# Kernel optimization log

Measured on AMD Instinct MI355X. Metric: run time of the kernel, lower is better.

Reference implementation:

```python
import jax, jax.numpy as jnp
import numpy as np

B, D, K, U = 4096, 1024, 5, 1024  # batch, input_dim, num_basis, units


def setup_inputs() -> dict:
    key = jax.random.key(0)
    k1, k2, k3 = jax.random.split(key, 3)
    x = jax.random.normal(k1, (B, D), dtype=jnp.float32)
    basis_weights = jax.random.normal(k2, (D, K, U), dtype=jnp.float32) * 0.02
    bias = jax.random.normal(k3, (U,), dtype=jnp.float32) * 0.02
    return {"x": x, "basis_weights": basis_weights, "bias": bias}


def reference(x, basis_weights, bias):
    # Polynomial basis expansion: x^0, x^1, ..., x^{K-1}  -> (B, D, K)
    num_basis = basis_weights.shape[1]
    powers = jnp.arange(num_basis, dtype=x.dtype)
    basis = x[..., None] ** powers  # x**0 == 1, matching tf.ones_like branch
    # Fused: einsum('bik,ikj->bij') followed by reduce_sum over i == 'bik,ikj->bj'.
    # Avoids materializing the (B, D, U) intermediate of the original.
    out = jnp.einsum("bik,ikj->bj", basis, basis_weights) + bias
    # tf.nn.gelu defaults to exact (non-approximate) GELU.
    return jax.nn.gelu(out, approximate=False)
```

## Files before the change

### kernel.cpp

```cpp
#include <hip/hip_runtime.h>
#include <hip/hip_bf16.h>
#include <math.h>


#define B_DIM 4096
#define D_DIM 1024
#define U_DIM 1024
#define KT2 4096
#define NKB 128

typedef unsigned short ushort_t;
typedef __attribute__((ext_vector_type(8))) short bf16x8;
typedef __attribute__((ext_vector_type(4))) float f32x4;

__device__ __forceinline__ ushort_t f2bf(float f) {
  union { float f; unsigned int u; } v;
  v.f = f;
  unsigned int r = v.u + 0x7FFFu + ((v.u >> 16) & 1u);
  return (ushort_t)(r >> 16);
}

__device__ __forceinline__ void load_lds16(const ushort_t* g, ushort_t* l) {
  __builtin_amdgcn_global_load_lds(
      (const __attribute__((address_space(1))) ushort_t*)g,
      (__attribute__((address_space(3))) ushort_t*)l, 16, 0, 0);
}

__device__ __forceinline__ float gelu_exact(float v) {
  return 0.5f * v * (1.0f + erff(v * 0.70710678118654752f));
}


__global__ __launch_bounds__(256) void prep_kernel(
    const float* __restrict__ x, const float* __restrict__ W,
    const float* __restrict__ bias, ushort_t* __restrict__ Ap,
    ushort_t* __restrict__ Bp, float* __restrict__ b2) {
  __shared__ __align__(16) float lsh[16][260];

  const int bid  = blockIdx.x;
  const int t    = threadIdx.x;
  const int wave = t >> 6;
  const int lane = t & 63;
  const int m    = lane & 15;
  const int ko   = lane >> 4;

  if (bid < 1024) {
    const int bx  = bid & 3;
    const int m16 = bid >> 2;
    const float* xbase = x + (size_t)m16 * 16 * D_DIM + bx * 256;
#pragma unroll
    for (int p = 0; p < 4; ++p) {
      const int row = p * 4 + wave;
      const int c4  = lane;
      *(float4*)&lsh[row][c4 * 4] =
          *(const float4*)(xbase + (size_t)row * D_DIM + c4 * 4);
    }
    __syncthreads();
#pragma unroll
    for (int u = 0; u < 8; ++u) {
      const int kl  = u * 4 + wave;
      const int col = kl * 8 + ko * 2;
      const float xa = lsh[m][col], xb = lsh[m][col + 1];
      const float xa2 = xa * xa, xb2 = xb * xb;
      ushort_t o[8];
      o[0] = f2bf(xa);  o[1] = f2bf(xa2);
      o[2] = f2bf(xa2 * xa); o[3] = f2bf(xa2 * xa2);
      o[4] = f2bf(xb);  o[5] = f2bf(xb2);
      o[6] = f2bf(xb2 * xb); o[7] = f2bf(xb2 * xb2);
      *(uint4*)(Ap + ((size_t)m16 * NKB + bx * 32 + kl) * 512 + lane * 8) =
          *(const uint4*)o;
    }
  } else {
    const int n16 = bid - 1024;
    const int j   = n16 * 16 + m;
    float s0 = 0.0f;
#pragma unroll 2
    for (int it2 = 0; it2 < 32; ++it2) {
      const int kblk = it2 * 4 + wave;
      const int i0   = kblk * 8 + ko * 2;
      ushort_t o[8];
#pragma unroll
      for (int t2 = 0; t2 < 2; ++t2) {
        const int i = i0 + t2;
        s0 += W[(size_t)(i * 5) * U_DIM + j];
#pragma unroll
        for (int e = 0; e < 4; ++e)
          o[t2 * 4 + e] = f2bf(W[(size_t)(i * 5 + e + 1) * U_DIM + j]);
      }
      *(uint4*)(Bp + ((size_t)n16 * NKB + kblk) * 512 + lane * 8) =
          *(const uint4*)o;
    }
    s0 += __shfl_xor(s0, 16, 64);
    s0 += __shfl_xor(s0, 32, 64);
    float* red = &lsh[0][0];
    __syncthreads();
    if (ko == 0) red[wave * 16 + m] = s0;
    __syncthreads();
    if (wave == 0 && ko == 0)
      b2[j] = bias[j] + red[m] + red[16 + m] + red[32 + m] + red[48 + m];
  }
}

__global__ __launch_bounds__(256) void gemm_kernel(
    const ushort_t* __restrict__ Ap, const ushort_t* __restrict__ Bp,
    const float* __restrict__ b2, float* __restrict__ C) {
  __shared__ __align__(16) ushort_t lds[4][12 * 512];

  const int tid  = threadIdx.x;
  const int wave = tid >> 6;
  const int lane = tid & 63;
  const int wm   = wave >> 1;
  const int wn   = wave & 1;

  const int lin  = blockIdx.y * 8 + blockIdx.x;
  const int xcd  = lin & 7;
  const int slot = lin >> 3;
  const int mt   = xcd * 8 + (slot & 7);
  const int nt   = slot >> 3;
  const int m16b = mt * 4;
  const int n16b = nt * 8;

  const ushort_t* gcur[3];
  int ldst[3];
#pragma unroll
  for (int s = 0; s < 3; ++s) {
    const int u = s * 4 + wave;
    const ushort_t* base = (u < 4)
        ? Ap + ((size_t)(m16b + u) * NKB) * 512
        : Bp + ((size_t)(n16b + (u - 4)) * NKB) * 512;
    gcur[s] = base + lane * 8;
    ldst[s] = u * 512 + lane * 8;
  }

  f32x4 acc[2][4];
  const f32x4 zero = {0.0f, 0.0f, 0.0f, 0.0f};
#pragma unroll
  for (int mf = 0; mf < 2; ++mf)
#pragma unroll
    for (int nf = 0; nf < 4; ++nf) acc[mf][nf] = zero;

#define WAITBAR(N) \
  asm volatile("s_waitcnt vmcnt(" #N ")\n\ts_barrier" ::: "memory")

#define STAGE_REL(bb, rel)                                              \
  do {                                                                  \
    _Pragma("unroll")                                                   \
    for (int s = 0; s < 3; ++s)                                         \
      load_lds16(gcur[s] + (rel) * 512, &lds[bb][ldst[s]]);             \
  } while (0)

#define COMPUTE(bb)                                                     \
  do {                                                                  \
    bf16x8 a[2], b[4];                                                  \
    _Pragma("unroll")                                                   \
    for (int mf = 0; mf < 2; ++mf)                                      \
      a[mf] = *(const bf16x8*)&lds[bb][(wm * 2 + mf) * 512 + lane * 8]; \
    _Pragma("unroll")                                                   \
    for (int nf = 0; nf < 4; ++nf)                                      \
      b[nf] = *(const bf16x8*)&lds[bb][(4 + wn * 4 + nf) * 512 + lane * 8]; \
    _Pragma("unroll")                                                   \
    for (int mf = 0; mf < 2; ++mf)                                      \
      _Pragma("unroll")                                                 \
      for (int nf = 0; nf < 4; ++nf)                                    \
        acc[mf][nf] = __builtin_amdgcn_mfma_f32_16x16x32_bf16(          \
            a[mf], b[nf], acc[mf][nf], 0, 0, 0);                        \
  } while (0)

  STAGE_REL(0, 0);
  STAGE_REL(1, 1);
  STAGE_REL(2, 2);
#pragma unroll
  for (int s = 0; s < 3; ++s) gcur[s] += 4 * 512;

  for (int base = 0; base < 124; base += 4) {
    WAITBAR(6); STAGE_REL(3, -1); COMPUTE(0);
    WAITBAR(6); STAGE_REL(0,  0); COMPUTE(1);
    WAITBAR(6); STAGE_REL(1,  1); COMPUTE(2);
    WAITBAR(6); STAGE_REL(2,  2); COMPUTE(3);
#pragma unroll
    for (int s = 0; s < 3; ++s) gcur[s] += 4 * 512;
  }
  WAITBAR(6); STAGE_REL(3, -1); COMPUTE(0);
  WAITBAR(6); COMPUTE(1);
  WAITBAR(3); COMPUTE(2);
  WAITBAR(0); COMPUTE(3);
#undef STAGE_REL
#undef COMPUTE
#undef WAITBAR

  const int crow0 = m16b * 16 + wm * 32 + (lane >> 4) * 4;
  const int ccol0 = n16b * 16 + wn * 64 + (lane & 15);
#pragma unroll
  for (int nf = 0; nf < 4; ++nf) {
    const int col = ccol0 + nf * 16;
    const float bv = b2[col];
#pragma unroll
    for (int mf = 0; mf < 2; ++mf) {
#pragma unroll
      for (int r = 0; r < 4; ++r) {
        const int row = crow0 + mf * 16 + r;
        C[(size_t)row * U_DIM + col] = gelu_exact(acc[mf][nf][r] + bv);
      }
    }
  }
}

__global__ void fallback_kernel(const float* __restrict__ x, const float* __restrict__ W,
                                const float* __restrict__ bias, float* __restrict__ out) {
  int j  = blockIdx.x * 256 + threadIdx.x;
  int b0 = blockIdx.y * 16;
  float acc[16];
#pragma unroll
  for (int t = 0; t < 16; ++t) acc[t] = 0.0f;
  for (int i = 0; i < D_DIM; ++i) {
    const float* wr = W + (size_t)i * 5 * U_DIM + j;
    float w0 = wr[0 * U_DIM], w1 = wr[1 * U_DIM], w2 = wr[2 * U_DIM];
    float w3 = wr[3 * U_DIM], w4 = wr[4 * U_DIM];
#pragma unroll
    for (int t = 0; t < 16; ++t) {
      float xv = x[(size_t)(b0 + t) * D_DIM + i];
      float x2 = xv * xv;
      acc[t] += w0 + xv * w1 + x2 * w2 + x2 * xv * w3 + x2 * x2 * w4;
    }
  }
  float bv = bias[j];
#pragma unroll
  for (int t = 0; t < 16; ++t)
    out[(size_t)(b0 + t) * U_DIM + j] = gelu_exact(acc[t] + bv);
}

extern "C" void kernel_launch(void* const* d_in, const int* in_sizes, int n_in,
                              void* d_out, int out_size, void* d_ws, size_t ws_size,
                              hipStream_t stream) {
  const float* x    = (const float*)d_in[0];
  const float* W    = (const float*)d_in[1];
  const float* bias = (const float*)d_in[2];
  float* out = (float*)d_out;

  const size_t szA = (size_t)B_DIM * KT2 * sizeof(ushort_t);
  const size_t szB = (size_t)U_DIM * KT2 * sizeof(ushort_t);
  const size_t szb = (size_t)U_DIM * sizeof(float);

  if (ws_size >= szA + szB + szb) {
    ushort_t* Ap = (ushort_t*)d_ws;
    ushort_t* Bp = (ushort_t*)((char*)d_ws + szA);
    float*    b2 = (float*)((char*)d_ws + szA + szB);
    prep_kernel<<<dim3(1024 + 64), 256, 0, stream>>>(x, W, bias, Ap, Bp, b2);
    gemm_kernel<<<dim3(U_DIM / 128, B_DIM / 64), 256, 0, stream>>>(Ap, Bp, b2, out);
  } else {
    fallback_kernel<<<dim3(U_DIM / 256, B_DIM / 16), 256, 0, stream>>>(x, W, bias, out);
  }
}
```

Before: 138.2 us.

## Compute polynomial powers of x inside GEMM instead of materializing bf16 A

The prep kernel now only relayouts x as fp32 into the MFMA fragment order. The GEMM loads two fp32 values per lane and computes x, x^2, x^3, x^4 and their bf16 packing on the fly, which shrinks the prep write and GEMM read of A from a 4x-expanded bf16 buffer to fp32 x. The W repack is split across 8 k-groups for more parallelism, with partial row-0 sums folded into the bias inside the GEMM epilogue. The cost is extra VALU work per MFMA step inside the GEMM main loop and a per-lane LDS read pattern that may cause bank conflicts.

Result: slower. 149.6 us (+8.2%).

```diff
diff --git a/kernel.cpp b/kernel.cpp
--- a/kernel.cpp
+++ b/kernel.cpp
@@ -6,12 +6,12 @@
 #define B_DIM 4096
 #define D_DIM 1024
 #define U_DIM 1024
-#define KT2 4096
 #define NKB 128
 
 typedef unsigned short ushort_t;
 typedef __attribute__((ext_vector_type(8))) short bf16x8;
 typedef __attribute__((ext_vector_type(4))) float f32x4;
+typedef __attribute__((ext_vector_type(2))) float f32x2;
 
 __device__ __forceinline__ ushort_t f2bf(float f) {
   union { float f; unsigned int u; } v;
@@ -33,9 +33,9 @@
 
 __global__ __launch_bounds__(256) void prep_kernel(
     const float* __restrict__ x, const float* __restrict__ W,
-    const float* __restrict__ bias, ushort_t* __restrict__ Ap,
-    ushort_t* __restrict__ Bp, float* __restrict__ b2) {
-  __shared__ __align__(16) float lsh[16][260];
+    float* __restrict__ Xp, ushort_t* __restrict__ Bp,
+    float* __restrict__ fold8) {
+  __shared__ __align__(16) float lsh[64][132];
 
   const int bid  = blockIdx.x;
   const int t    = threadIdx.x;
@@ -44,39 +44,38 @@
   const int m    = lane & 15;
   const int ko   = lane >> 4;
 
-  if (bid < 1024) {
-    const int bx  = bid & 3;
-    const int m16 = bid >> 2;
-    const float* xbase = x + (size_t)m16 * 16 * D_DIM + bx * 256;
-#pragma unroll
-    for (int p = 0; p < 4; ++p) {
-      const int row = p * 4 + wave;
-      const int c4  = lane;
+  if (bid < 512) {
+    const int mt = bid >> 3;
+    const int g  = bid & 7;
+    const float* xbase = x + (size_t)mt * 64 * D_DIM + g * 128;
+#pragma unroll
+    for (int p = 0; p < 8; ++p) {
+      const int row = p * 8 + wave * 2 + (lane >> 5);
+      const int c4  = lane & 31;
       *(float4*)&lsh[row][c4 * 4] =
           *(const float4*)(xbase + (size_t)row * D_DIM + c4 * 4);
     }
     __syncthreads();
 #pragma unroll
-    for (int u = 0; u < 8; ++u) {
-      const int kl  = u * 4 + wave;
-      const int col = kl * 8 + ko * 2;
-      const float xa = lsh[m][col], xb = lsh[m][col + 1];
-      const float xa2 = xa * xa, xb2 = xb * xb;
-      ushort_t o[8];
-      o[0] = f2bf(xa);  o[1] = f2bf(xa2);
-      o[2] = f2bf(xa2 * xa); o[3] = f2bf(xa2 * xa2);
-      o[4] = f2bf(xb);  o[5] = f2bf(xb2);
-      o[6] = f2bf(xb2 * xb); o[7] = f2bf(xb2 * xb2);
-      *(uint4*)(Ap + ((size_t)m16 * NKB + bx * 32 + kl) * 512 + lane * 8) =
-          *(const uint4*)o;
+    for (int r = 0; r < 4; ++r) {
+      const int itl = r * 4 + wave;
+      const int it  = g * 16 + itl;
+      float* dst = Xp + ((size_t)(mt * NKB + it)) * 512 + lane * 8;
+      float f[8];
+#pragma unroll
+      for (int j = 0; j < 8; ++j) f[j] = lsh[lane][itl * 8 + j];
+      *(float4*)(dst)     = *(const float4*)&f[0];
+      *(float4*)(dst + 4) = *(const float4*)&f[4];
     }
   } else {
-    const int n16 = bid - 1024;
+    const int wid = bid - 512;
+    const int n16 = wid >> 3;
+    const int kg  = wid & 7;
     const int j   = n16 * 16 + m;
     float s0 = 0.0f;
-#pragma unroll 2
-    for (int it2 = 0; it2 < 32; ++it2) {
-      const int kblk = it2 * 4 + wave;
+#pragma unroll
+    for (int kk = 0; kk < 4; ++kk) {
+      const int kblk = kg * 16 + kk * 4 + wave;
       const int i0   = kblk * 8 + ko * 2;
       ushort_t o[8];
 #pragma unroll
@@ -93,18 +92,19 @@
     s0 += __shfl_xor(s0, 16, 64);
     s0 += __shfl_xor(s0, 32, 64);
     float* red = &lsh[0][0];
-    __syncthreads();
     if (ko == 0) red[wave * 16 + m] = s0;
     __syncthreads();
     if (wave == 0 && ko == 0)
-      b2[j] = bias[j] + red[m] + red[16 + m] + red[32 + m] + red[48 + m];
+      fold8[(size_t)kg * U_DIM + j] =
+          red[m] + red[16 + m] + red[32 + m] + red[48 + m];
   }
 }
 
 __global__ __launch_bounds__(256) void gemm_kernel(
-    const ushort_t* __restrict__ Ap, const ushort_t* __restrict__ Bp,
-    const float* __restrict__ b2, float* __restrict__ C) {
-  __shared__ __align__(16) ushort_t lds[4][12 * 512];
+    const float* __restrict__ Xp, const ushort_t* __restrict__ Bp,
+    const float* __restrict__ bias, const float* __restrict__ fold8,
+    float* __restrict__ C) {
+  __shared__ __align__(16) ushort_t lds[4][5120];
 
   const int tid  = threadIdx.x;
   const int wave = tid >> 6;
@@ -120,17 +120,13 @@
   const int m16b = mt * 4;
   const int n16b = nt * 8;
 
-  const ushort_t* gcur[3];
-  int ldst[3];
-#pragma unroll
-  for (int s = 0; s < 3; ++s) {
-    const int u = s * 4 + wave;
-    const ushort_t* base = (u < 4)
-        ? Ap + ((size_t)(m16b + u) * NKB) * 512
-        : Bp + ((size_t)(n16b + (u - 4)) * NKB) * 512;
-    gcur[s] = base + lane * 8;
-    ldst[s] = u * 512 + lane * 8;
-  }
+  const ushort_t* gx  = (const ushort_t*)(Xp + (size_t)mt * NKB * 512) + lane * 8;
+  const ushort_t* gb0 = Bp + ((size_t)(n16b + wave) * NKB) * 512 + lane * 8;
+  const ushort_t* gb1 = Bp + ((size_t)(n16b + 4 + wave) * NKB) * 512 + lane * 8;
+  const int ldx0 = lane * 8;
+  const int ldx1 = 512 + lane * 8;
+  const int ldb0 = 1024 + wave * 512 + lane * 8;
+  const int ldb1 = 1024 + (4 + wave) * 512 + lane * 8;
 
   f32x4 acc[2][4];
   const f32x4 zero = {0.0f, 0.0f, 0.0f, 0.0f};
@@ -144,20 +140,37 @@
 
 #define STAGE_REL(bb, rel)                                              \
   do {                                                                  \
-    _Pragma("unroll")                                                   \
-    for (int s = 0; s < 3; ++s)                                         \
-      load_lds16(gcur[s] + (rel) * 512, &lds[bb][ldst[s]]);             \
+    load_lds16(gx  + (rel) * 1024,       &lds[bb][ldx0]);               \
+    load_lds16(gx  + (rel) * 1024 + 512, &lds[bb][ldx1]);               \
+    load_lds16(gb0 + (rel) * 512,        &lds[bb][ldb0]);               \
+    load_lds16(gb1 + (rel) * 512,        &lds[bb][ldb1]);               \
+  } while (0)
+
+#define PACKA(dst, xp)                                                  \
+  do {                                                                  \
+    const f32x2 p1 = (xp);                                              \
+    const f32x2 p2 = p1 * p1;                                           \
+    const f32x2 p3 = p2 * p1;                                           \
+    const f32x2 p4 = p2 * p2;                                           \
+    bf16x8 rr;                                                          \
+    rr[0] = (short)f2bf(p1[0]); rr[1] = (short)f2bf(p2[0]);             \
+    rr[2] = (short)f2bf(p3[0]); rr[3] = (short)f2bf(p4[0]);             \
+    rr[4] = (short)f2bf(p1[1]); rr[5] = (short)f2bf(p2[1]);             \
+    rr[6] = (short)f2bf(p3[1]); rr[7] = (short)f2bf(p4[1]);             \
+    dst = rr;                                                           \
   } while (0)
 
 #define COMPUTE(bb)                                                     \
   do {                                                                  \
+    const float* xu = (const float*)&lds[bb][0];                        \
+    f32x2 xp0 = *(const f32x2*)&xu[((wm * 2 + 0) * 16 + (lane & 15)) * 8 + (lane >> 4) * 2]; \
+    f32x2 xp1 = *(const f32x2*)&xu[((wm * 2 + 1) * 16 + (lane & 15)) * 8 + (lane >> 4) * 2]; \
     bf16x8 a[2], b[4];                                                  \
-    _Pragma("unroll")                                                   \
-    for (int mf = 0; mf < 2; ++mf)                                      \
-      a[mf] = *(const bf16x8*)&lds[bb][(wm * 2 + mf) * 512 + lane * 8]; \
+    PACKA(a[0], xp0);                                                   \
+    PACKA(a[1], xp1);                                                   \
     _Pragma("unroll")                                                   \
     for (int nf = 0; nf < 4; ++nf)                                      \
-      b[nf] = *(const bf16x8*)&lds[bb][(4 + wn * 4 + nf) * 512 + lane * 8]; \
+      b[nf] = *(const bf16x8*)&lds[bb][1024 + (wn * 4 + nf) * 512 + lane * 8]; \
     _Pragma("unroll")                                                   \
     for (int mf = 0; mf < 2; ++mf)                                      \
       _Pragma("unroll")                                                 \
@@ -169,23 +182,26 @@
   STAGE_REL(0, 0);
   STAGE_REL(1, 1);
   STAGE_REL(2, 2);
-#pragma unroll
-  for (int s = 0; s < 3; ++s) gcur[s] += 4 * 512;
+  gx  += 4 * 1024;
+  gb0 += 4 * 512;
+  gb1 += 4 * 512;
 
   for (int base = 0; base < 124; base += 4) {
-    WAITBAR(6); STAGE_REL(3, -1); COMPUTE(0);
-    WAITBAR(6); STAGE_REL(0,  0); COMPUTE(1);
-    WAITBAR(6); STAGE_REL(1,  1); COMPUTE(2);
-    WAITBAR(6); STAGE_REL(2,  2); COMPUTE(3);
-#pragma unroll
-    for (int s = 0; s < 3; ++s) gcur[s] += 4 * 512;
-  }
-  WAITBAR(6); STAGE_REL(3, -1); COMPUTE(0);
-  WAITBAR(6); COMPUTE(1);
-  WAITBAR(3); COMPUTE(2);
+    WAITBAR(8); STAGE_REL(3, -1); COMPUTE(0);
+    WAITBAR(8); STAGE_REL(0,  0); COMPUTE(1);
+    WAITBAR(8); STAGE_REL(1,  1); COMPUTE(2);
+    WAITBAR(8); STAGE_REL(2,  2); COMPUTE(3);
+    gx  += 4 * 1024;
+    gb0 += 4 * 512;
+    gb1 += 4 * 512;
+  }
+  WAITBAR(8); STAGE_REL(3, -1); COMPUTE(0);
+  WAITBAR(8); COMPUTE(1);
+  WAITBAR(4); COMPUTE(2);
   WAITBAR(0); COMPUTE(3);
 #undef STAGE_REL
 #undef COMPUTE
+#undef PACKA
 #undef WAITBAR
 
   const int crow0 = m16b * 16 + wm * 32 + (lane >> 4) * 4;
@@ -193,7 +209,9 @@
 #pragma unroll
   for (int nf = 0; nf < 4; ++nf) {
     const int col = ccol0 + nf * 16;
-    const float bv = b2[col];
+    float bv = bias[col];
+#pragma unroll
+    for (int kg = 0; kg < 8; ++kg) bv += fold8[(size_t)kg * U_DIM + col];
 #pragma unroll
     for (int mf = 0; mf < 2; ++mf) {
 #pragma unroll
@@ -237,16 +255,16 @@
   const float* bias = (const float*)d_in[2];
   float* out = (float*)d_out;
 
-  const size_t szA = (size_t)B_DIM * KT2 * sizeof(ushort_t);
-  const size_t szB = (size_t)U_DIM * KT2 * sizeof(ushort_t);
-  const size_t szb = (size_t)U_DIM * sizeof(float);
-
-  if (ws_size >= szA + szB + szb) {
-    ushort_t* Ap = (ushort_t*)d_ws;
-    ushort_t* Bp = (ushort_t*)((char*)d_ws + szA);
-    float*    b2 = (float*)((char*)d_ws + szA + szB);
-    prep_kernel<<<dim3(1024 + 64), 256, 0, stream>>>(x, W, bias, Ap, Bp, b2);
-    gemm_kernel<<<dim3(U_DIM / 128, B_DIM / 64), 256, 0, stream>>>(Ap, Bp, b2, out);
+  const size_t szX = (size_t)B_DIM * D_DIM * sizeof(float);
+  const size_t szB = (size_t)U_DIM * 4096 * sizeof(ushort_t);
+  const size_t szF = (size_t)8 * U_DIM * sizeof(float);
+
+  if (ws_size >= szX + szB + szF) {
+    float*    Xp = (float*)d_ws;
+    ushort_t* Bp = (ushort_t*)((char*)d_ws + szX);
+    float*    f8 = (float*)((char*)d_ws + szX + szB);
+    prep_kernel<<<dim3(1024), 256, 0, stream>>>(x, W, Xp, Bp, f8);
+    gemm_kernel<<<dim3(U_DIM / 128, B_DIM / 64), 256, 0, stream>>>(Xp, Bp, bias, f8, out);
   } else {
     fallback_kernel<<<dim3(U_DIM / 256, B_DIM / 16), 256, 0, stream>>>(x, W, bias, out);
   }
```
